# Kernel optimization log

Hardware: AMD Instinct MI355X
Metric: run time of the kernel (lower is better)

## Reference

```python
import jax, jax.numpy as jnp
import numpy as np

N_NODES = 50000
N_EDGES = 400000
IN_DIM = 4
HID = 32
NCLASSES = 4
N_ITERS = 3


def setup_inputs() -> dict:
    key = jax.random.key(0)
    ks = jax.random.split(key, 8)

    def w(k, shape, fan_in):
        return (jax.random.normal(k, shape, dtype=jnp.float32) / np.sqrt(fan_in)).astype(jnp.float32)

    x = jax.random.normal(ks[0], (3, N_NODES, IN_DIM), dtype=jnp.float32)
    edge_index = jax.random.randint(ks[1], (3, 2, N_EDGES), 0, N_NODES, dtype=jnp.int64)
    hi = HID + IN_DIM  # 36: feats of m = cat([H, X])
    return {
        "x": x,
        "edge_index": edge_index,
        "in_W": w(ks[2], (3, IN_DIM, HID), IN_DIM),
        "in_b": jnp.zeros((3, HID), jnp.float32),
        "eW1": w(ks[3], (3, 2 * hi, HID), 2 * hi),
        "eb1": jnp.zeros((3, HID), jnp.float32),
        "eW2": w(ks[4], (3, HID, 1), HID),
        "eb2": jnp.zeros((3, 1), jnp.float32),
        "nW1": w(ks[5], (3, 3 * hi, HID), 3 * hi),
        "nb1": jnp.zeros((3, HID), jnp.float32),
        "nW2": w(ks[6], (3, HID, HID), HID),
        "nb2": jnp.zeros((3, HID), jnp.float32),
    }


def _forward(x, edge_index, in_W, in_b, eW1, eb1, eW2, eb2, nW1, nb1, nW2, nb2):
    n_nodes = x.shape[1]

    def edge_net(j, m, row, col):
        # B: [E, C, 2*(h+in)] -- detached in the original module
        B = jax.lax.stop_gradient(jnp.concatenate([m[col], m[row]], axis=-1))
        t = jnp.tanh(B @ eW1[j] + eb1[j])
        t = jnp.tanh(t @ eW2[j] + eb2[j])  # [E, C, 1]
        return jax.nn.softmax(t, axis=1)  # softmax over class dim

    def node_net(j, m, ea, row, col):
        mi = jax.ops.segment_sum(ea * m[row], col, num_segments=n_nodes)
        mo = jax.ops.segment_sum(ea * m[col], row, num_segments=n_nodes)
        M = jnp.concatenate([mi, mo, m], axis=-1)  # [N, C, 3*(h+in)]
        t = jnp.tanh(M @ nW1[j] + nb1[j])
        return jnp.tanh(t @ nW2[j] + nb2[j])  # [N, C, hid]

    rows = [edge_index[j, 0] for j in range(3)]
    cols = [edge_index[j, 1] for j in range(3)]
    # X: node feats repeated per class, [N, C, in]
    X = [jnp.broadcast_to(x[j][:, None, :], (n_nodes, NCLASSES, x.shape[-1])) for j in range(3)]
    H = [jnp.tanh(X[j] @ in_W[j] + in_b[j]) for j in range(3)]
    m = [jnp.concatenate([H[j], X[j]], axis=-1) for j in range(3)]

    for _ in range(N_ITERS):
        for j in range(3):
            ea = edge_net(j, m[j], rows[j], cols[j])
            H[j] = node_net(j, m[j], ea, rows[j], cols[j])
        m = [jnp.concatenate([H[j], X[j]], axis=-1) for j in range(3)]

    # classify_node=False: final edge-network pass per plane, squeeze -> [E, C]
    ret = [edge_net(j, m[j], rows[j], cols[j])[..., 0] for j in range(3)]
    return jnp.concatenate(ret, axis=0)  # [3*E, C]


def reference(x, edge_index, in_W, in_b, eW1, eb1, eW2, eb2, nW1, nb1, nW2, nb2):
    return _forward(x, edge_index, in_W, in_b, eW1, eb1, eW2, eb2, nW1, nb1, nW2, nb2)
```

## Files before the change

kernel.cpp:

```cpp
#include <hip/hip_runtime.h>
#include <hip/hip_fp16.h>

#define N_NODES 50000
#define N_EDGES 400000
#define NCLS 4
#define HID 32
#define HI 36
#define ROWS_P (N_NODES * NCLS)
#define PADCAP 672000
#define SLICES 8
#define BUCKS_PER_SLICE (N_NODES / SLICES)
#define NCHUNKS ((N_NODES + 255) / 256)

__device__ __forceinline__ float fast_tanh(float x) {
    float e = __builtin_amdgcn_exp2f(x * 2.885390081777927f);
    float r = __builtin_amdgcn_rcpf(1.0f + e);
    return fmaf(-2.0f, r, 1.0f);
}

#if __has_builtin(__builtin_amdgcn_fdot2)
typedef _Float16 h2v __attribute__((ext_vector_type(2)));
__device__ __forceinline__ float fdot2f(__half2 a, __half2 b, float c) {
    return __builtin_amdgcn_fdot2(__builtin_bit_cast(h2v, a),
                                  __builtin_bit_cast(h2v, b), c, false);
}
#else
__device__ __forceinline__ float fdot2f(__half2 a, __half2 b, float c) {
    float2 af = __half22float2(a), bf = __half22float2(b);
    return c + af.x * bf.x + af.y * bf.y;
}
#endif

union F4H8 { float4 f4; __half2 h2[4]; };
union F2H4 { float2 f2; __half2 h2[2]; };

__global__ void k_init(const float* __restrict__ x, const float* __restrict__ W,
                       const float* __restrict__ b, __half* __restrict__ m) {
    unsigned t = blockIdx.x * 256 + threadIdx.x;
    if (t >= N_NODES * HI) return;
    unsigned idx = t % HI;
    unsigned n   = t / HI;
    float x0 = x[n * 4 + 0], x1 = x[n * 4 + 1];
    float x2 = x[n * 4 + 2], x3 = x[n * 4 + 3];
    float val;
    if (idx < 32) {
        float a = b[idx];
        a += x0 * W[idx] + x1 * W[32 + idx] + x2 * W[64 + idx] + x3 * W[96 + idx];
        val = fast_tanh(a);
    } else {
        val = (idx == 32) ? x0 : (idx == 33) ? x1 : (idx == 34) ? x2 : x3;
    }
    __half hv = __float2half_rn(val);
    __half* dst = m + (size_t)n * (NCLS * HI) + idx;
    dst[0] = hv; dst[HI] = hv; dst[2 * HI] = hv; dst[3 * HI] = hv;
}

__global__ void k_pass1(const int* __restrict__ rowI, const int* __restrict__ colI,
                        int* __restrict__ inCnt, int* __restrict__ outCnt,
                        int* __restrict__ tmpLi) {
    unsigned e = blockIdx.x * 256 + threadIdx.x;
    if (e >= N_EDGES) return;
    int r = rowI[e], cn = colI[e];
    int liIn  = atomicAdd(&inCnt[cn], 1);
    int liOut = atomicAdd(&outCnt[r], 1);
    tmpLi[e] = liIn | (liOut << 16);
}

__global__ void k_scanA(const int* __restrict__ inCnt, const int* __restrict__ outCnt,
                        int* __restrict__ bsum) {
    unsigned v = blockIdx.x / NCHUNKS, chunk = blockIdx.x % NCHUNKS;
    unsigned i = chunk * 256 + threadIdx.x;
    const int* cnt = (v == 2) ? outCnt : inCnt;
    int val = (i < N_NODES) ? cnt[i] : 0;
    if (v) val = (val + 7) & ~7;
#pragma unroll
    for (int d = 1; d < 64; d <<= 1) val += __shfl_xor(val, d, 64);
    __shared__ int sh[4];
    unsigned lane = threadIdx.x & 63, wid = threadIdx.x >> 6;
    if (lane == 0) sh[wid] = val;
    __syncthreads();
    if (threadIdx.x == 0) bsum[blockIdx.x] = sh[0] + sh[1] + sh[2] + sh[3];
}

__global__ void k_scanB(const int* __restrict__ bsum, int* __restrict__ boff,
                        int* __restrict__ offs) {
    unsigned v = blockIdx.x;
    int tid = threadIdx.x;
    int val = (tid < NCHUNKS) ? bsum[v * NCHUNKS + tid] : 0;
    int lane = tid & 63, wid = tid >> 6;
    int incl = val;
#pragma unroll
    for (int d = 1; d < 64; d <<= 1) {
        int t = __shfl_up(incl, d, 64);
        if (lane >= d) incl += t;
    }
    __shared__ int sh[4];
    if (lane == 63) sh[wid] = incl;
    __syncthreads();
    int waveOff = (wid == 0) ? 0 : (wid == 1) ? sh[0] :
                  (wid == 2) ? sh[0] + sh[1] : sh[0] + sh[1] + sh[2];
    incl += waveOff;
    if (tid < NCHUNKS) boff[v * NCHUNKS + tid] = incl - val;
    if (tid == NCHUNKS - 1) offs[(size_t)v * (N_NODES + 1) + N_NODES] = incl;
}

__global__ void k_scanC(const int* __restrict__ inCnt, const int* __restrict__ outCnt,
                        const int* __restrict__ boff, int* __restrict__ offs) {
    unsigned v = blockIdx.x / NCHUNKS, chunk = blockIdx.x % NCHUNKS;
    unsigned i = chunk * 256 + threadIdx.x;
    const int* cnt = (v == 2) ? outCnt : inCnt;
    int val = (i < N_NODES) ? cnt[i] : 0;
    if (v) val = (val + 7) & ~7;
    int lane = threadIdx.x & 63, wid = threadIdx.x >> 6;
    int incl = val;
#pragma unroll
    for (int d = 1; d < 64; d <<= 1) {
        int t = __shfl_up(incl, d, 64);
        if (lane >= d) incl += t;
    }
    __shared__ int sh[4];
    if (lane == 63) sh[wid] = incl;
    __syncthreads();
    int waveOff = (wid == 0) ? 0 : (wid == 1) ? sh[0] :
                  (wid == 2) ? sh[0] + sh[1] : sh[0] + sh[1] + sh[2];
    if (i < N_NODES)
        offs[(size_t)v * (N_NODES + 1) + i] = boff[v * NCHUNKS + chunk] + incl + waveOff - val;
}

__global__ void k_pass2(const int* __restrict__ rowI, const int* __restrict__ colI,
                        const int* __restrict__ tmpLi,
                        const int* __restrict__ inOffRaw, const int* __restrict__ pinOff,
                        const int* __restrict__ poutOff,
                        int4* __restrict__ edgeRec,
                        unsigned short* __restrict__ inPrt,
                        unsigned short* __restrict__ outPrt) {
    unsigned b = blockIdx.x;
    unsigned slice = b & (SLICES - 1);
    unsigned e = (b >> 3) * 256 + threadIdx.x;
    if (e >= N_EDGES) return;
    int r = rowI[e], cn = colI[e];
    int li = tmpLi[e];
    int liIn  = li & 0xFFFF;
    int liOut = (int)(((unsigned)li) >> 16);
    unsigned lo = slice * BUCKS_PER_SLICE;
    if ((unsigned)(cn - lo) < BUCKS_PER_SLICE) {
        int dense = inOffRaw[cn] + liIn;
        int piP   = pinOff[cn] + liIn;
        int poP   = poutOff[r] + liOut;
        edgeRec[dense] = make_int4(r | (cn << 16), piP, poP, (int)e);
        inPrt[piP] = (unsigned short)r;
    }
    if ((unsigned)(r - lo) < BUCKS_PER_SLICE) {
        int poP = poutOff[r] + liOut;
        outPrt[poP] = (unsigned short)cn;
    }
}


__global__ void k_gemm5(const __half* __restrict__ m,
                        const float* __restrict__ eW1, const float* __restrict__ nW1,
                        const float* __restrict__ eb1, const float* __restrict__ nb1,
                        __half* __restrict__ u, __half* __restrict__ v,
                        __half* __restrict__ p, __half* __restrict__ q,
                        __half* __restrict__ r) {
    constexpr int RPB = 32;
    __shared__ __half sm[RPB * 40];
    unsigned tid = threadIdx.x;
    unsigned r0  = blockIdx.x * RPB;
    if (tid < RPB * 9) {
        uint2 d = reinterpret_cast<const uint2*>(m + (size_t)r0 * HI)[tid];
        unsigned row = tid / 9, off = tid % 9;
        *reinterpret_cast<uint2*>(sm + row * 40 + off * 4) = d;
    }
    unsigned o = tid % 160, grp = tid / 160;
    unsigned sub = o >> 5, oo = o & 31;
    const float* W = (sub == 0) ? eW1 : (sub == 1) ? eW1 + 36 * 32 :
                     (sub == 2) ? nW1 : (sub == 3) ? nW1 + 36 * 32 : nW1 + 72 * 32;
    __half* dsth   = (sub == 0) ? u : (sub == 1) ? v : (sub == 2) ? p :
                     (sub == 3) ? q : r;
    float bias = (sub == 0) ? eb1[oo] : (sub == 4) ? nb1[oo] : 0.f;
    __half2 wc[18];
#pragma unroll
    for (int t = 0; t < 18; ++t)
        wc[t] = __floats2half2_rn(W[(2 * t) * 32 + oo], W[(2 * t + 1) * 32 + oo]);
    __syncthreads();
#pragma unroll
    for (int i = 0; i < 16; ++i) {
        unsigned rloc = grp * 16 + i;
        const __half* rowp = sm + rloc * 40;
        F4H8 A0, A1, A2, A3; F2H4 A4;
        A0.f4 = *reinterpret_cast<const float4*>(rowp);
        A1.f4 = *reinterpret_cast<const float4*>(rowp + 8);
        A2.f4 = *reinterpret_cast<const float4*>(rowp + 16);
        A3.f4 = *reinterpret_cast<const float4*>(rowp + 24);
        A4.f2 = *reinterpret_cast<const float2*>(rowp + 32);
        float acc = bias;
#pragma unroll
        for (int t = 0; t < 4; ++t) acc = fdot2f(A0.h2[t], wc[t], acc);
#pragma unroll
        for (int t = 0; t < 4; ++t) acc = fdot2f(A1.h2[t], wc[4 + t], acc);
#pragma unroll
        for (int t = 0; t < 4; ++t) acc = fdot2f(A2.h2[t], wc[8 + t], acc);
#pragma unroll
        for (int t = 0; t < 4; ++t) acc = fdot2f(A3.h2[t], wc[12 + t], acc);
        acc = fdot2f(A4.h2[0], wc[16], acc);
        acc = fdot2f(A4.h2[1], wc[17], acc);
        dsth[(size_t)(r0 + rloc) * 32 + oo] = __float2half_rn(acc);
    }
}

__global__ void k_gemm2(const __half* __restrict__ m, const float* __restrict__ W0,
                        const float* __restrict__ W1, const float* __restrict__ eb1,
                        __half* __restrict__ o0, __half* __restrict__ o1) {
    constexpr int RPB = 32;
    __shared__ __half sm[RPB * 40];
    unsigned tid = threadIdx.x;
    unsigned r0  = blockIdx.x * RPB;
    for (unsigned i = tid; i < RPB * 9; i += 256) {
        uint2 d = reinterpret_cast<const uint2*>(m + (size_t)r0 * HI)[i];
        unsigned row = i / 9, off = i % 9;
        *reinterpret_cast<uint2*>(sm + row * 40 + off * 4) = d;
    }
    unsigned o = tid % 64, grp = tid / 64;
    unsigned sub = o >> 5, oo = o & 31;
    const float* W = sub ? W1 : W0;
    __half* dst    = sub ? o1 : o0;
    float bias = sub ? 0.f : eb1[oo];
    __half2 wc[18];
#pragma unroll
    for (int t = 0; t < 18; ++t)
        wc[t] = __floats2half2_rn(W[(2 * t) * 32 + oo], W[(2 * t + 1) * 32 + oo]);
    __syncthreads();
#pragma unroll
    for (int i = 0; i < 8; ++i) {
        unsigned rloc = grp * 8 + i;
        const __half* rowp = sm + rloc * 40;
        F4H8 A0, A1, A2, A3; F2H4 A4;
        A0.f4 = *reinterpret_cast<const float4*>(rowp);
        A1.f4 = *reinterpret_cast<const float4*>(rowp + 8);
        A2.f4 = *reinterpret_cast<const float4*>(rowp + 16);
        A3.f4 = *reinterpret_cast<const float4*>(rowp + 24);
        A4.f2 = *reinterpret_cast<const float2*>(rowp + 32);
        float acc = bias;
#pragma unroll
        for (int t = 0; t < 4; ++t) acc = fdot2f(A0.h2[t], wc[t], acc);
#pragma unroll
        for (int t = 0; t < 4; ++t) acc = fdot2f(A1.h2[t], wc[4 + t], acc);
#pragma unroll
        for (int t = 0; t < 4; ++t) acc = fdot2f(A2.h2[t], wc[8 + t], acc);
#pragma unroll
        for (int t = 0; t < 4; ++t) acc = fdot2f(A3.h2[t], wc[12 + t], acc);
        acc = fdot2f(A4.h2[0], wc[16], acc);
        acc = fdot2f(A4.h2[1], wc[17], acc);
        dst[(size_t)(r0 + rloc) * 32 + oo] = __float2half_rn(acc);
    }
}

template <bool FINAL>
__global__ void k_edge(const int4* __restrict__ edgeRec,
                       const __half* __restrict__ u, const __half* __restrict__ v,
                       const float* __restrict__ w2, const float* __restrict__ b2,
                       __half* __restrict__ eaIn, __half* __restrict__ eaOut,
                       float* __restrict__ dst) {
    unsigned nwg = gridDim.x, bid = blockIdx.x;
    unsigned qq = nwg >> 3, rr = nwg & 7;
    unsigned xcd = bid & 7, loc = bid >> 3;
    unsigned swz = (xcd < rr ? xcd * (qq + 1) : rr * (qq + 1) + (xcd - rr) * qq) + loc;
    unsigned g   = swz * 256 + threadIdx.x;
    unsigned c   = g & 3;
    unsigned idx = g >> 2;
    int4 rec = edgeRec[idx];
    unsigned rc  = (unsigned)rec.x;
    unsigned row = rc & 0xFFFFu, col = rc >> 16;
    const float4* u4 = reinterpret_cast<const float4*>(u + (col * 4 + c) * 32);
    const float4* v4 = reinterpret_cast<const float4*>(v + (row * 4 + c) * 32);
    float t2 = b2[0];
#pragma unroll
    for (int i = 0; i < 4; ++i) {
        F4H8 U, V; U.f4 = u4[i]; V.f4 = v4[i];
#pragma unroll
        for (int jj = 0; jj < 4; ++jj) {
            float2 sf = __half22float2(__hadd2(U.h2[jj], V.h2[jj]));
            int o = i * 8 + jj * 2;
            t2 += fast_tanh(sf.x) * w2[o];
            t2 += fast_tanh(sf.y) * w2[o + 1];
        }
    }
    float s  = fast_tanh(t2);
    float m1 = fmaxf(s, __shfl_xor(s, 1, 4));
    float mx = fmaxf(m1, __shfl_xor(m1, 2, 4));
    float ex = __expf(s - mx);
    float sm = ex + __shfl_xor(ex, 1, 4);
    sm = sm + __shfl_xor(sm, 2, 4);
    float val = ex * __builtin_amdgcn_rcpf(sm);
    if (FINAL) {
        dst[(unsigned)rec.w * 4 + c] = val;
    } else {
        __half hv = __float2half_rn(val);
        eaIn[(size_t)c * PADCAP + (unsigned)rec.y] = hv;
        eaOut[(size_t)c * PADCAP + (unsigned)rec.z] = hv;
    }
}

__global__ void __launch_bounds__(64, 4)
k_node(__half* __restrict__ m, const __half* __restrict__ rbuf,
       const __half* __restrict__ p, const __half* __restrict__ q,
       const __half* __restrict__ eaInT, const __half* __restrict__ eaOutT,
       const int* __restrict__ pinOff, const int* __restrict__ poutOff,
       const unsigned short* __restrict__ inPrt,
       const unsigned short* __restrict__ outPrt,
       const float* __restrict__ nW2, const float* __restrict__ nb2) {
    unsigned lane = threadIdx.x;
    unsigned c2 = lane >> 5, k = lane & 31;
    unsigned n = blockIdx.x;
    unsigned gOff0 = c2 * 32 + k;
    unsigned gOff1 = gOff0 + 64;

    float h0 = __half2float(rbuf[((size_t)n * 4 + c2) * 32 + k]);
    float h1 = __half2float(rbuf[((size_t)n * 4 + c2 + 2) * 32 + k]);

    int bi0 = pinOff[n],  biE = pinOff[n + 1];
    int bo0 = poutOff[n], boE = poutOff[n + 1];
    __builtin_assume((bi0 & 7) == 0);
    __builtin_assume((bo0 & 7) == 0);

    const __half* eaI0 = eaInT + (size_t)c2 * PADCAP;
    const __half* eaI1 = eaInT + (size_t)(c2 + 2) * PADCAP;
    const __half* eaO0 = eaOutT + (size_t)c2 * PADCAP;
    const __half* eaO1 = eaOutT + (size_t)(c2 + 2) * PADCAP;

    auto accum = [&](const __half* __restrict__ base, uint4 prtv, uint4 e0v, uint4 e1v) {
        unsigned pr0 = prtv.x & 0xFFFFu, pr1 = prtv.x >> 16;
        unsigned pr2 = prtv.y & 0xFFFFu, pr3 = prtv.y >> 16;
        unsigned pr4 = prtv.z & 0xFFFFu, pr5 = prtv.z >> 16;
        unsigned pr6 = prtv.w & 0xFFFFu, pr7 = prtv.w >> 16;
        __half g0h[8], g1h[8];
        const __half* r0p = base + (size_t)pr0 * 128u; g0h[0] = r0p[gOff0]; g1h[0] = r0p[gOff1];
        const __half* r1p = base + (size_t)pr1 * 128u; g0h[1] = r1p[gOff0]; g1h[1] = r1p[gOff1];
        const __half* r2p = base + (size_t)pr2 * 128u; g0h[2] = r2p[gOff0]; g1h[2] = r2p[gOff1];
        const __half* r3p = base + (size_t)pr3 * 128u; g0h[3] = r3p[gOff0]; g1h[3] = r3p[gOff1];
        const __half* r4p = base + (size_t)pr4 * 128u; g0h[4] = r4p[gOff0]; g1h[4] = r4p[gOff1];
        const __half* r5p = base + (size_t)pr5 * 128u; g0h[5] = r5p[gOff0]; g1h[5] = r5p[gOff1];
        const __half* r6p = base + (size_t)pr6 * 128u; g0h[6] = r6p[gOff0]; g1h[6] = r6p[gOff1];
        const __half* r7p = base + (size_t)pr7 * 128u; g0h[7] = r7p[gOff0]; g1h[7] = r7p[gOff1];
        union { uint4 u4; __half2 h2[4]; } E0, E1;
        E0.u4 = e0v; E1.u4 = e1v;
#pragma unroll
        for (int ii = 0; ii < 4; ++ii) {
            h0 = fdot2f(E0.h2[ii], __halves2half2(g0h[2 * ii], g0h[2 * ii + 1]), h0);
            h1 = fdot2f(E1.h2[ii], __halves2half2(g1h[2 * ii], g1h[2 * ii + 1]), h1);
        }
    };

    uint4 oprt = {0, 0, 0, 0}, oe0 = {0, 0, 0, 0}, oe1 = {0, 0, 0, 0};
    if (bo0 < boE) {
        oprt = *(const uint4*)(outPrt + bo0);
        oe0  = *(const uint4*)(eaO0 + bo0);
        oe1  = *(const uint4*)(eaO1 + bo0);
    }

    if (bi0 < biE) {
        uint4 cprt = *(const uint4*)(inPrt + bi0);
        uint4 ce0  = *(const uint4*)(eaI0 + bi0);
        uint4 ce1  = *(const uint4*)(eaI1 + bi0);
        for (int b = bi0; b < biE; b += 8) {
            uint4 nprt = cprt, ne0 = ce0, ne1 = ce1;
            if (b + 8 < biE) {
                nprt = *(const uint4*)(inPrt + b + 8);
                ne0  = *(const uint4*)(eaI0 + b + 8);
                ne1  = *(const uint4*)(eaI1 + b + 8);
            }
            accum(p, cprt, ce0, ce1);
            cprt = nprt; ce0 = ne0; ce1 = ne1;
        }
    }
    if (bo0 < boE) {
        uint4 cprt = oprt, ce0 = oe0, ce1 = oe1;
        for (int b = bo0; b < boE; b += 8) {
            uint4 nprt = cprt, ne0 = ce0, ne1 = ce1;
            if (b + 8 < boE) {
                nprt = *(const uint4*)(outPrt + b + 8);
                ne0  = *(const uint4*)(eaO0 + b + 8);
                ne1  = *(const uint4*)(eaO1 + b + 8);
            }
            accum(q, cprt, ce0, ce1);
            cprt = nprt; ce0 = ne0; ce1 = ne1;
        }
    }

    float t0 = fast_tanh(h0);
    float t1 = fast_tanh(h1);
    float hh0 = nb2[k], hh1 = hh0;
#pragma unroll
    for (int kk = 0; kk < 32; ++kk) {
        float w = nW2[kk * 32 + k];
        float s0 = __shfl(t0, (int)(c2 * 32 + kk), 64);
        float s1 = __shfl(t1, (int)(c2 * 32 + kk), 64);
        hh0 += s0 * w;
        hh1 += s1 * w;
    }
    m[((size_t)n * 4 + c2) * HI + k]     = __float2half_rn(fast_tanh(hh0));
    m[((size_t)n * 4 + c2 + 2) * HI + k] = __float2half_rn(fast_tanh(hh1));
}

extern "C" void kernel_launch(void* const* d_in, const int* in_sizes, int n_in,
                              void* d_out, int out_size, void* d_ws, size_t ws_size,
                              hipStream_t stream) {
    const float* x   = (const float*)d_in[0];
    const int*   ei  = (const int*)d_in[1];
    const float* inW = (const float*)d_in[2];
    const float* inb = (const float*)d_in[3];
    const float* eW1 = (const float*)d_in[4];
    const float* eb1 = (const float*)d_in[5];
    const float* eW2 = (const float*)d_in[6];
    const float* eb2 = (const float*)d_in[7];
    const float* nW1 = (const float*)d_in[8];
    const float* nb1 = (const float*)d_in[9];
    const float* nW2 = (const float*)d_in[10];
    const float* nb2 = (const float*)d_in[11];
    float* out = (float*)d_out;

    __half* m     = (__half*)d_ws;
    __half* u     = m + (size_t)ROWS_P * HI;
    __half* v     = u + (size_t)ROWS_P * 32;
    __half* p     = v + (size_t)ROWS_P * 32;
    __half* q     = p + (size_t)ROWS_P * 32;
    __half* rbuf  = q + (size_t)ROWS_P * 32;
    __half* eaIn  = rbuf + (size_t)ROWS_P * 32;
    __half* eaOut = eaIn + (size_t)PADCAP * 4;
    unsigned short* inPrt  = (unsigned short*)(eaOut + (size_t)PADCAP * 4);
    unsigned short* outPrt = inPrt + PADCAP;
    int4*   edgeRec = (int4*)(outPrt + PADCAP);
    int*    inOffRaw = (int*)(edgeRec + N_EDGES);
    int*    pinOff   = inOffRaw + (N_NODES + 1);
    int*    poutOff  = pinOff + (N_NODES + 1);
    int*    inCnt    = poutOff + (N_NODES + 1);
    int*    outCnt   = inCnt + N_NODES;
    int*    bsum     = outCnt + N_NODES;
    int*    boff     = bsum + 3 * NCHUNKS;
    int*    tmpLi    = (int*)u;

    const int gridE = (N_EDGES + 255) / 256;
    const size_t zeroBytes = (size_t)PADCAP * 4 * 2 * 2 + (size_t)PADCAP * 2 * 2;

    for (int j = 0; j < 3; ++j) {
        const int*   rowI = ei + (size_t)j * 2 * N_EDGES;
        const int*   colI = rowI + N_EDGES;
        const float* eW1j = eW1 + j * 72 * 32;
        const float* eb1j = eb1 + j * 32;
        const float* eW2j = eW2 + j * 32;
        const float* eb2j = eb2 + j;
        const float* nW1j = nW1 + j * 108 * 32;
        const float* nb1j = nb1 + j * 32;
        const float* nW2j = nW2 + j * 1024;
        const float* nb2j = nb2 + j * 32;

        hipMemsetAsync(inCnt, 0, 2 * N_NODES * sizeof(int), stream);
        hipMemsetAsync(eaIn, 0, zeroBytes, stream);
        k_pass1<<<gridE, 256, 0, stream>>>(rowI, colI, inCnt, outCnt, tmpLi);
        k_scanA<<<3 * NCHUNKS, 256, 0, stream>>>(inCnt, outCnt, bsum);
        k_scanB<<<3, 256, 0, stream>>>(bsum, boff, inOffRaw);
        k_scanC<<<3 * NCHUNKS, 256, 0, stream>>>(inCnt, outCnt, boff, inOffRaw);
        k_pass2<<<gridE * SLICES, 256, 0, stream>>>(rowI, colI, tmpLi,
                                                    inOffRaw, pinOff, poutOff,
                                                    edgeRec, inPrt, outPrt);

        k_init<<<(N_NODES * HI + 255) / 256, 256, 0, stream>>>(
            x + (size_t)j * N_NODES * 4, inW + j * 128, inb + j * 32, m);

        for (int it = 0; it < 3; ++it) {
            k_gemm5<<<ROWS_P / 32, 320, 0, stream>>>(m, eW1j, nW1j, eb1j, nb1j,
                                                     u, v, p, q, rbuf);
            k_edge<false><<<N_EDGES * 4 / 256, 256, 0, stream>>>(
                edgeRec, u, v, eW2j, eb2j, eaIn, eaOut, nullptr);
            k_node<<<N_NODES, 64, 0, stream>>>(m, rbuf, p, q, eaIn, eaOut,
                                               pinOff, poutOff, inPrt, outPrt,
                                               nW2j, nb2j);
        }
        k_gemm2<<<ROWS_P / 32, 256, 0, stream>>>(m, eW1j, eW1j + 36 * 32, eb1j, u, v);
        k_edge<true><<<N_EDGES * 4 / 256, 256, 0, stream>>>(
            edgeRec, u, v, eW2j, eb2j, nullptr, nullptr,
            out + (size_t)j * N_EDGES * 4);
    }
}
```

Before: 1.454 ms.

## Batch CSR construction for all three planes into single kernel launches

```diff
diff --git a/kernel.cpp b/kernel.cpp
--- a/kernel.cpp
+++ b/kernel.cpp
@@ -11,6 +11,15 @@
 #define SLICES 8
 #define BUCKS_PER_SLICE (N_NODES / SLICES)
 #define NCHUNKS ((N_NODES + 255) / 256)
+#define GRIDE ((N_EDGES + 255) / 256)
+
+#define OFF_EREC 0
+#define OFF_OFFS 1600000
+#define OFF_CNT  1750003
+#define OFF_BSUM 1850003
+#define OFF_BOFF 1850591
+#define OFF_PRT  1851180
+#define CSR_STRIDE 2523180
 
 __device__ __forceinline__ float fast_tanh(float x) {
     float e = __builtin_amdgcn_exp2f(x * 2.885390081777927f);
@@ -55,22 +64,29 @@
     dst[0] = hv; dst[HI] = hv; dst[2 * HI] = hv; dst[3 * HI] = hv;
 }
 
-__global__ void k_pass1(const int* __restrict__ rowI, const int* __restrict__ colI,
-                        int* __restrict__ inCnt, int* __restrict__ outCnt,
+__global__ void k_pass1(const int* __restrict__ ei, int* __restrict__ csr,
                         int* __restrict__ tmpLi) {
-    unsigned e = blockIdx.x * 256 + threadIdx.x;
+    unsigned jj = blockIdx.x / GRIDE;
+    unsigned e  = (blockIdx.x % GRIDE) * 256 + threadIdx.x;
     if (e >= N_EDGES) return;
+    const int* rowI = ei + (size_t)jj * 2 * N_EDGES;
+    const int* colI = rowI + N_EDGES;
+    int* base   = csr + (size_t)jj * CSR_STRIDE;
+    int* inCnt  = base + OFF_CNT;
+    int* outCnt = inCnt + N_NODES;
     int r = rowI[e], cn = colI[e];
     int liIn  = atomicAdd(&inCnt[cn], 1);
     int liOut = atomicAdd(&outCnt[r], 1);
-    tmpLi[e] = liIn | (liOut << 16);
-}
-
-__global__ void k_scanA(const int* __restrict__ inCnt, const int* __restrict__ outCnt,
-                        int* __restrict__ bsum) {
-    unsigned v = blockIdx.x / NCHUNKS, chunk = blockIdx.x % NCHUNKS;
+    tmpLi[(size_t)jj * N_EDGES + e] = liIn | (liOut << 16);
+}
+
+__global__ void k_scanA(int* __restrict__ csr) {
+    unsigned jj  = blockIdx.x / (3 * NCHUNKS);
+    unsigned rem = blockIdx.x % (3 * NCHUNKS);
+    unsigned v = rem / NCHUNKS, chunk = rem % NCHUNKS;
+    int* base = csr + (size_t)jj * CSR_STRIDE;
+    const int* cnt = base + OFF_CNT + (v == 2 ? N_NODES : 0);
     unsigned i = chunk * 256 + threadIdx.x;
-    const int* cnt = (v == 2) ? outCnt : inCnt;
     int val = (i < N_NODES) ? cnt[i] : 0;
     if (v) val = (val + 7) & ~7;
 #pragma unroll
@@ -79,12 +95,15 @@
     unsigned lane = threadIdx.x & 63, wid = threadIdx.x >> 6;
     if (lane == 0) sh[wid] = val;
     __syncthreads();
-    if (threadIdx.x == 0) bsum[blockIdx.x] = sh[0] + sh[1] + sh[2] + sh[3];
-}
-
-__global__ void k_scanB(const int* __restrict__ bsum, int* __restrict__ boff,
-                        int* __restrict__ offs) {
-    unsigned v = blockIdx.x;
+    if (threadIdx.x == 0) (base + OFF_BSUM)[rem] = sh[0] + sh[1] + sh[2] + sh[3];
+}
+
+__global__ void k_scanB(int* __restrict__ csr) {
+    unsigned jj = blockIdx.x / 3, v = blockIdx.x % 3;
+    int* base = csr + (size_t)jj * CSR_STRIDE;
+    const int* bsum = base + OFF_BSUM;
+    int* boff = base + OFF_BOFF;
+    int* offs = base + OFF_OFFS;
     int tid = threadIdx.x;
     int val = (tid < NCHUNKS) ? bsum[v * NCHUNKS + tid] : 0;
     int lane = tid & 63, wid = tid >> 6;
@@ -104,11 +123,15 @@
     if (tid == NCHUNKS - 1) offs[(size_t)v * (N_NODES + 1) + N_NODES] = incl;
 }
 
-__global__ void k_scanC(const int* __restrict__ inCnt, const int* __restrict__ outCnt,
-                        const int* __restrict__ boff, int* __restrict__ offs) {
-    unsigned v = blockIdx.x / NCHUNKS, chunk = blockIdx.x % NCHUNKS;
+__global__ void k_scanC(int* __restrict__ csr) {
+    unsigned jj  = blockIdx.x / (3 * NCHUNKS);
+    unsigned rem = blockIdx.x % (3 * NCHUNKS);
+    unsigned v = rem / NCHUNKS, chunk = rem % NCHUNKS;
+    int* base = csr + (size_t)jj * CSR_STRIDE;
+    const int* cnt = base + OFF_CNT + (v == 2 ? N_NODES : 0);
+    const int* boff = base + OFF_BOFF;
+    int* offs = base + OFF_OFFS;
     unsigned i = chunk * 256 + threadIdx.x;
-    const int* cnt = (v == 2) ? outCnt : inCnt;
     int val = (i < N_NODES) ? cnt[i] : 0;
     if (v) val = (val + 7) & ~7;
     int lane = threadIdx.x & 63, wid = threadIdx.x >> 6;
@@ -127,19 +150,24 @@
         offs[(size_t)v * (N_NODES + 1) + i] = boff[v * NCHUNKS + chunk] + incl + waveOff - val;
 }
 
-__global__ void k_pass2(const int* __restrict__ rowI, const int* __restrict__ colI,
-                        const int* __restrict__ tmpLi,
-                        const int* __restrict__ inOffRaw, const int* __restrict__ pinOff,
-                        const int* __restrict__ poutOff,
-                        int4* __restrict__ edgeRec,
-                        unsigned short* __restrict__ inPrt,
-                        unsigned short* __restrict__ outPrt) {
-    unsigned b = blockIdx.x;
-    unsigned slice = b & (SLICES - 1);
-    unsigned e = (b >> 3) * 256 + threadIdx.x;
+__global__ void k_pass2(const int* __restrict__ ei, int* __restrict__ csr,
+                        const int* __restrict__ tmpLi) {
+    unsigned jj  = blockIdx.x / (GRIDE * SLICES);
+    unsigned rem = blockIdx.x % (GRIDE * SLICES);
+    unsigned slice = rem & (SLICES - 1);
+    unsigned e = (rem >> 3) * 256 + threadIdx.x;
     if (e >= N_EDGES) return;
+    const int* rowI = ei + (size_t)jj * 2 * N_EDGES;
+    const int* colI = rowI + N_EDGES;
+    int* base = csr + (size_t)jj * CSR_STRIDE;
+    const int* inOffRaw = base + OFF_OFFS;
+    const int* pinOff   = inOffRaw + (N_NODES + 1);
+    const int* poutOff  = pinOff + (N_NODES + 1);
+    int4* edgeRec = (int4*)(base + OFF_EREC);
+    unsigned short* inPrt  = (unsigned short*)(base + OFF_PRT);
+    unsigned short* outPrt = inPrt + PADCAP;
     int r = rowI[e], cn = colI[e];
-    int li = tmpLi[e];
+    int li = tmpLi[(size_t)jj * N_EDGES + e];
     int liIn  = li & 0xFFFF;
     int liOut = (int)(((unsigned)li) >> 16);
     unsigned lo = slice * BUCKS_PER_SLICE;
@@ -428,24 +456,30 @@
     __half* rbuf  = q + (size_t)ROWS_P * 32;
     __half* eaIn  = rbuf + (size_t)ROWS_P * 32;
     __half* eaOut = eaIn + (size_t)PADCAP * 4;
-    unsigned short* inPrt  = (unsigned short*)(eaOut + (size_t)PADCAP * 4);
-    unsigned short* outPrt = inPrt + PADCAP;
-    int4*   edgeRec = (int4*)(outPrt + PADCAP);
-    int*    inOffRaw = (int*)(edgeRec + N_EDGES);
-    int*    pinOff   = inOffRaw + (N_NODES + 1);
-    int*    poutOff  = pinOff + (N_NODES + 1);
-    int*    inCnt    = poutOff + (N_NODES + 1);
-    int*    outCnt   = inCnt + N_NODES;
-    int*    bsum     = outCnt + N_NODES;
-    int*    boff     = bsum + 3 * NCHUNKS;
-    int*    tmpLi    = (int*)u;
-
-    const int gridE = (N_EDGES + 255) / 256;
-    const size_t zeroBytes = (size_t)PADCAP * 4 * 2 * 2 + (size_t)PADCAP * 2 * 2;
+    int*    csr   = (int*)(eaOut + (size_t)PADCAP * 4);
+    int*    tmpLi = (int*)u;
+
+    const size_t csrBaseBytes = (size_t)((char*)csr - (char*)d_ws);
+    const bool merged = ws_size >= csrBaseBytes + 3u * (size_t)CSR_STRIDE * 4 + 256;
+
+    const size_t zeroEA  = (size_t)PADCAP * 4 * 2 * 2;
+    const size_t cntB    = (size_t)2 * N_NODES * 4;
+    const size_t prtB    = (size_t)2 * PADCAP * 2;
+
+    if (merged) {
+        for (int j = 0; j < 3; ++j) {
+            int* bj = csr + (size_t)j * CSR_STRIDE;
+            hipMemsetAsync(bj + OFF_CNT, 0, cntB, stream);
+            hipMemsetAsync(bj + OFF_PRT, 0, prtB, stream);
+        }
+        k_pass1<<<3 * GRIDE, 256, 0, stream>>>(ei, csr, tmpLi);
+        k_scanA<<<9 * NCHUNKS, 256, 0, stream>>>(csr);
+        k_scanB<<<9, 256, 0, stream>>>(csr);
+        k_scanC<<<9 * NCHUNKS, 256, 0, stream>>>(csr);
+        k_pass2<<<3 * GRIDE * SLICES, 256, 0, stream>>>(ei, csr, tmpLi);
+    }
 
     for (int j = 0; j < 3; ++j) {
-        const int*   rowI = ei + (size_t)j * 2 * N_EDGES;
-        const int*   colI = rowI + N_EDGES;
         const float* eW1j = eW1 + j * 72 * 32;
         const float* eb1j = eb1 + j * 32;
         const float* eW2j = eW2 + j * 32;
@@ -455,16 +489,24 @@
         const float* nW2j = nW2 + j * 1024;
         const float* nb2j = nb2 + j * 32;
 
-        hipMemsetAsync(inCnt, 0, 2 * N_NODES * sizeof(int), stream);
-        hipMemsetAsync(eaIn, 0, zeroBytes, stream);
-        k_pass1<<<gridE, 256, 0, stream>>>(rowI, colI, inCnt, outCnt, tmpLi);
-        k_scanA<<<3 * NCHUNKS, 256, 0, stream>>>(inCnt, outCnt, bsum);
-        k_scanB<<<3, 256, 0, stream>>>(bsum, boff, inOffRaw);
-        k_scanC<<<3 * NCHUNKS, 256, 0, stream>>>(inCnt, outCnt, boff, inOffRaw);
-        k_pass2<<<gridE * SLICES, 256, 0, stream>>>(rowI, colI, tmpLi,
-                                                    inOffRaw, pinOff, poutOff,
-                                                    edgeRec, inPrt, outPrt);
-
+        int* bj = csr + (merged ? (size_t)j * CSR_STRIDE : 0);
+        if (!merged) {
+            hipMemsetAsync(bj + OFF_CNT, 0, cntB, stream);
+            hipMemsetAsync(bj + OFF_PRT, 0, prtB, stream);
+            k_pass1<<<GRIDE, 256, 0, stream>>>(ei + (size_t)j * 2 * N_EDGES, bj, tmpLi);
+            k_scanA<<<3 * NCHUNKS, 256, 0, stream>>>(bj);
+            k_scanB<<<3, 256, 0, stream>>>(bj);
+            k_scanC<<<3 * NCHUNKS, 256, 0, stream>>>(bj);
+            k_pass2<<<GRIDE * SLICES, 256, 0, stream>>>(ei + (size_t)j * 2 * N_EDGES,
+                                                        bj, tmpLi);
+        }
+        const int4* edgeRec = (const int4*)(bj + OFF_EREC);
+        const int*  pinOff  = bj + OFF_OFFS + (N_NODES + 1);
+        const int*  poutOff = bj + OFF_OFFS + 2 * (N_NODES + 1);
+        const unsigned short* inPrt  = (const unsigned short*)(bj + OFF_PRT);
+        const unsigned short* outPrt = inPrt + PADCAP;
+
+        hipMemsetAsync(eaIn, 0, zeroEA, stream);
         k_init<<<(N_NODES * HI + 255) / 256, 256, 0, stream>>>(
             x + (size_t)j * N_NODES * 4, inW + j * 128, inb + j * 32, m);
 
```

Result: no change. 1.440 ms, median of 2 (-1.0%).
